# Kernel tuning notes

Measured on AMD Instinct MI355X. Metric: run time of the kernel, lower is better.

Reference implementation:

```python
import jax, jax.numpy as jnp
import numpy as np

N_FFT = 4096
HOP = 1024
EPS = 1e-10


def hann(n):
    # periodic Hann window, matches torch.hann_window(n)
    return 0.5 - 0.5 * jnp.cos(2.0 * jnp.pi * jnp.arange(n) / n)


def stft(x, window):
    # x: (..., T) real -> (..., F, frames) complex; center=True, reflect pad, onesided
    pad = N_FFT // 2
    x = jnp.pad(x, [(0, 0)] * (x.ndim - 1) + [(pad, pad)], mode='reflect')
    n_frames = 1 + (x.shape[-1] - N_FFT) // HOP
    idx = jnp.arange(n_frames)[:, None] * HOP + jnp.arange(N_FFT)[None, :]
    frames = x[..., idx] * window  # (..., frames, N_FFT)
    return jnp.swapaxes(jnp.fft.rfft(frames, axis=-1), -1, -2)  # (..., F, frames)


def istft(spec, window, length):
    # spec: (..., F, frames) complex -> (..., length) real; torch.istft semantics (center=True)
    frames = jnp.fft.irfft(jnp.swapaxes(spec, -1, -2), n=N_FFT, axis=-1) * window
    n_frames = frames.shape[-2]
    out_len = N_FFT + HOP * (n_frames - 1)
    idx = (jnp.arange(n_frames)[:, None] * HOP + jnp.arange(N_FFT)[None, :]).reshape(-1)
    flat = frames.reshape(frames.shape[:-2] + (-1,))
    y = jnp.zeros(frames.shape[:-2] + (out_len,), frames.dtype).at[..., idx].add(flat)
    wsq = jnp.zeros((out_len,), frames.dtype).at[idx].add(jnp.tile(window ** 2, n_frames))
    y = y / jnp.where(wsq > 1e-11, wsq, 1.0)
    pad = N_FFT // 2
    return y[..., pad:pad + length]


def setup_inputs() -> dict:
    key = jax.random.key(0)
    k1, k2, k3 = jax.random.split(key, 3)
    audio = jax.random.normal(k1, (2, 2, 441000), jnp.float32)
    W = jax.random.normal(k2, (4, 2049, 2049), jnp.float32) * 0.02
    b = jax.random.normal(k3, (4, 2049), jnp.float32) * 0.01
    return {"audio": audio, "W": W, "b": b}


def reference(audio, W, b):
    window = hann(N_FFT).astype(audio.dtype)
    mix = stft(audio, window)                 # (N, C, F, T) complex64
    X = jnp.abs(mix)                          # ComplexNorm, mono=False, power=1
    Xd = jax.lax.stop_gradient(X)             # Separator feeds X.detach() to target models
    # target models: per-target linear over frequency bins + ReLU (nonneg spectrogram)
    V = jax.nn.relu(jnp.einsum('ncft,jgf->njcgt', Xd, W) + b[None, :, None, :, None])
    # wiener(iterations=0, softmask=False, residual=False): y_j = v_j * exp(i*angle(mix))
    phase = mix / (jnp.abs(mix) + EPS)        # unit-magnitude complex
    Y = V.astype(phase.real.dtype) * phase[:, None]  # (N, J, C, F, T) complex
    estimates = istft(Y, window, audio.shape[-1])    # (N, J, C, T_audio)
    return estimates
```

## Files before the change

### kernel.cpp

```cpp
#include <hip/hip_runtime.h>
#include <hip/hip_bf16.h>
#include <math.h>

#define T_AUDIO 441000
#define NH   2048
#define HOP  1024
#define NBINS 2049
#define NFRAMES 431
#define PAD  2048

#define GP  2176
#define KP  2112
#define TPN 448

#define NBLK 108
#define SPAN 7168

#define NSTFT (4 * NFRAMES)
#define NCONV ((4 * GP * KP / 8 + 255) / 256)

#define TWO_PI 6.2831853071795864769f

#define PADI(i) ((i) + ((i) >> 4))

typedef __bf16 bf16_t;
typedef bf16_t bf16x8 __attribute__((ext_vector_type(8)));
typedef bf16_t bf16x4 __attribute__((ext_vector_type(4)));
typedef float f32x4 __attribute__((ext_vector_type(4)));
typedef float f32x4u __attribute__((ext_vector_type(4), aligned(4)));
typedef _Float16 h16;
typedef h16 h16x2 __attribute__((ext_vector_type(2)));

__device__ __forceinline__ unsigned pack_bf2(float a, float b) {
    union { bf16_t h; unsigned short u; } ca, cb;
    ca.h = (bf16_t)a; cb.h = (bf16_t)b;
    return (unsigned)ca.u | ((unsigned)cb.u << 16);
}
__device__ __forceinline__ float2 unpack_bf2(unsigned v) {
    union { unsigned u; float f; } a, b;
    a.u = v << 16;
    b.u = v & 0xffff0000u;
    return make_float2(a.f, b.f);
}

__device__ __forceinline__ float2 cadd(float2 a, float2 b) { return make_float2(a.x + b.x, a.y + b.y); }
__device__ __forceinline__ float2 csub(float2 a, float2 b) { return make_float2(a.x - b.x, a.y - b.y); }
__device__ __forceinline__ float2 cmul(float2 a, float2 b) {
    return make_float2(a.x * b.x - a.y * b.y, a.x * b.y + a.y * b.x);
}
__device__ __forceinline__ float2 cmulc(float2 u, float2 w) {
    return make_float2(u.x * w.x + u.y * w.y, u.y * w.x - u.x * w.y);
}

__global__ void k_tab(float2* __restrict__ tw) {
    int i = blockIdx.x * 256 + threadIdx.x;
    if (i < 4096) {
        float s, c;
        sincosf((float)i * (TWO_PI / 4096.0f), &s, &c);
        tw[i] = make_float2(c, s);
    }
}


__device__ __forceinline__ void load_own(float2 v[8], const float2* x, int tid) {
    #pragma unroll
    for (int k = 0; k < 8; k++) v[k] = x[PADI(tid + 256 * k)];
}

template<bool FWD>
__device__ __forceinline__ void r8_sweep_store(const float2 v[8], float2* x,
        int tid, int s, int ls, int fac, const float2* __restrict__ tw) {
    const float sgn = FWD ? -1.0f : 1.0f;
    const float R2 = 0.70710678118654752440f;
    int q = tid & (s - 1);
    int p = tid >> ls;
    int e = p * fac;
    float2 w[7];
    #pragma unroll
    for (int k = 0; k < 7; k++) w[k] = tw[e * (k + 1)];
    float2 s0 = cadd(v[0], v[4]), s1 = cadd(v[1], v[5]),
           s2 = cadd(v[2], v[6]), s3 = cadd(v[3], v[7]);
    float2 d0 = csub(v[0], v[4]), d1 = csub(v[1], v[5]),
           d2 = csub(v[2], v[6]), d3 = csub(v[3], v[7]);
    float2 X0, X1, X2, X3, X4, X5, X6, X7;
    {
        float2 t0 = cadd(s0, s2), t1 = csub(s0, s2);
        float2 t2 = cadd(s1, s3), t3 = csub(s1, s3);
        float2 it3 = make_float2(-sgn * t3.y, sgn * t3.x);
        X0 = cadd(t0, t2); X4 = csub(t0, t2);
        X2 = cadd(t1, it3); X6 = csub(t1, it3);
    }
    {
        float2 e0 = d0;
        float2 e1 = make_float2(R2 * (d1.x - sgn * d1.y), R2 * (sgn * d1.x + d1.y));
        float2 e2 = make_float2(-sgn * d2.y, sgn * d2.x);
        float2 e3 = make_float2(-R2 * (d3.x + sgn * d3.y), R2 * (sgn * d3.x - d3.y));
        float2 t0 = cadd(e0, e2), t1 = csub(e0, e2);
        float2 t2 = cadd(e1, e3), t3 = csub(e1, e3);
        float2 it3 = make_float2(-sgn * t3.y, sgn * t3.x);
        X1 = cadd(t0, t2); X5 = csub(t0, t2);
        X3 = cadd(t1, it3); X7 = csub(t1, it3);
    }
    int ob = q + 8 * s * p;
    x[PADI(ob)] = X0;
    float2 XX[7] = {X1, X2, X3, X4, X5, X6, X7};
    #pragma unroll
    for (int k = 0; k < 7; k++) {
        float2 u = XX[k];
        x[PADI(ob + s * (k + 1))] = FWD ? cmulc(u, w[k]) : cmul(w[k], u);
    }
}

__device__ __forceinline__ void r4_final_reg(const float2 v[8], float2 o[8],
                                             float sgn) {
    #pragma unroll
    for (int h = 0; h < 2; h++) {
        float2 c0 = v[h], c1 = v[h + 2], c2 = v[h + 4], c3 = v[h + 6];
        float2 t0 = cadd(c0, c2), t1 = csub(c0, c2);
        float2 t2 = cadd(c1, c3), t3 = csub(c1, c3);
        float2 it3 = make_float2(-sgn * t3.y, sgn * t3.x);
        o[h]     = cadd(t0, t2);
        o[h + 2] = cadd(t1, it3);
        o[h + 4] = csub(t0, t2);
        o[h + 6] = csub(t1, it3);
    }
}

template<bool FWD>
__device__ __forceinline__ void fft_mid(float2 v[8], float2* buf, int tid,
                                        const float2* __restrict__ tw) {
    r8_sweep_store<FWD>(v, buf, tid, 1, 0, 2, tw);
    __syncthreads();
    load_own(v, buf, tid);
    __syncthreads();
    r8_sweep_store<FWD>(v, buf, tid, 8, 3, 16, tw);
    __syncthreads();
    load_own(v, buf, tid);
    __syncthreads();
    r8_sweep_store<FWD>(v, buf, tid, 64, 6, 128, tw);
    __syncthreads();
    load_own(v, buf, tid);
    __syncthreads();
}

__global__ __launch_bounds__(256) void k_prep(const float* __restrict__ audio,
        const float* __restrict__ W, bf16_t* __restrict__ Wb,
        bf16_t* __restrict__ Xb, unsigned* __restrict__ ph,
        const float2* __restrict__ tw) {
    __shared__ float2 buf[2176];
    int bid = blockIdx.x;
    int tid = threadIdx.x;
    if (bid >= NSTFT) {
        size_t idx = (size_t)(bid - NSTFT) * 256 + tid;
        size_t total = (size_t)4 * GP * KP / 8;
        if (idx >= total) return;
        size_t e = idx * 8;
        int f0 = (int)(e % KP);
        size_t rem = e / KP;
        int g = (int)(rem % GP);
        int j = (int)(rem / GP);
        bf16x8 v = {};
        if (g < NBINS) {
            const float* src = W + ((size_t)j * NBINS + g) * NBINS;
            if (f0 + 7 < NBINS) {
                f32x4u a0 = *(const f32x4u*)(src + f0);
                f32x4u a1 = *(const f32x4u*)(src + f0 + 4);
                #pragma unroll
                for (int r = 0; r < 4; r++) { v[r] = (bf16_t)a0[r]; v[r + 4] = (bf16_t)a1[r]; }
            } else {
                #pragma unroll
                for (int r = 0; r < 8; r++) {
                    int f = f0 + r;
                    v[r] = (bf16_t)(f < NBINS ? src[f] : 0.0f);
                }
            }
        }
        *(bf16x8*)(Wb + e) = v;
        return;
    }
    int nc = bid / NFRAMES;
    int fr = bid - nc * NFRAMES;
    const float* a = audio + (size_t)nc * T_AUDIO;
    int base = fr * HOP - PAD;
    float2 v[8];
    #pragma unroll
    for (int it = 0; it < 8; it++) {
        int m = tid + it * 256;
        int r0 = base + 2 * m;
        int r1 = r0 + 1;
        r0 = r0 < 0 ? -r0 : (r0 >= T_AUDIO ? 2 * T_AUDIO - 2 - r0 : r0);
        r1 = r1 < 0 ? -r1 : (r1 >= T_AUDIO ? 2 * T_AUDIO - 2 - r1 : r1);
        float4 tt = ((const float4*)tw)[m];
        v[it] = make_float2(a[r0] * (0.5f - 0.5f * tt.x),
                            a[r1] * (0.5f - 0.5f * tt.z));
    }
    fft_mid<true>(v, buf, tid, tw);
    {
        float2 o[8];
        r4_final_reg(v, o, -1.0f);
        #pragma unroll
        for (int it = 0; it < 8; it++) buf[PADI(tid + 256 * it)] = o[it];
    }
    __syncthreads();
    size_t orow = ((size_t)nc * NFRAMES + fr) * KP;
    bf16_t* Xrow = Xb + ((size_t)nc * TPN + fr) * KP;
    for (int k = tid; k < NBINS; k += 256) {
        float2 Zk = buf[PADI(k & 2047)];
        float2 Zm = buf[PADI((2048 - k) & 2047)];
        float ex = 0.5f * (Zk.x + Zm.x), ey = 0.5f * (Zk.y - Zm.y);
        float ox = 0.5f * (Zk.y + Zm.y), oy = -0.5f * (Zk.x - Zm.x);
        float2 w = tw[k];
        float re = ex + w.x * ox + w.y * oy;
        float im = ey + w.x * oy - w.y * ox;
        float mag = sqrtf(re * re + im * im);
        float inv = 1.0f / (mag + 1e-10f);
        Xrow[k] = (bf16_t)mag;
        ph[orow + k] = pack_bf2(re * inv, im * inv);
    }
}

__global__ __launch_bounds__(256) void k_gemm_mfma(const bf16_t* __restrict__ Wb,
        const float* __restrict__ bias, const bf16_t* __restrict__ Xb,
        bf16_t* __restrict__ V) {
    __shared__ bf16_t As[128 * 64];
    __shared__ bf16_t Bs[64 * 64];
    int id = blockIdx.x;
    int xcd = id & 7, nn = id >> 3;
    int G = xcd + 8 * (nn / 28);
    if (G >= 68) return;
    int m28 = nn % 28;
    int j  = G / 17;
    int g0 = (G % 17) * 128;
    int nc = m28 / 7;
    int t0 = (m28 % 7) * 64;
    const bf16_t* A = Wb + ((size_t)j * GP + g0) * KP;
    const bf16_t* B = Xb + ((size_t)nc * TPN + t0) * KP;
    int tid = threadIdx.x;
    int lane = tid & 63, wid = tid >> 6;
    int wm = wid >> 1, wn = wid & 1;

    const bf16_t* srcA[4];
    #pragma unroll
    for (int i = 0; i < 4; i++) {
        int s = i * 256 + tid;
        int r = s >> 3, cc = (s & 7) ^ (r & 7);
        srcA[i] = A + (size_t)r * KP + cc * 8;
    }
    const bf16_t* srcB[2];
    #pragma unroll
    for (int i = 0; i < 2; i++) {
        int s = i * 256 + tid;
        int r = s >> 3, cc = (s & 7) ^ (r & 7);
        srcB[i] = B + (size_t)r * KP + cc * 8;
    }

    int laneLo = lane & 15, laneHi = lane >> 4;
    int offA[4][2], offB[2][2];
    #pragma unroll
    for (int mm = 0; mm < 4; mm++) {
        int r = wm * 64 + mm * 16 + laneLo;
        #pragma unroll
        for (int kk = 0; kk < 2; kk++) {
            int c = kk * 4 + laneHi;
            offA[mm][kk] = r * 128 + ((c ^ (r & 7)) << 4);
        }
    }
    #pragma unroll
    for (int n = 0; n < 2; n++) {
        int r = wn * 32 + n * 16 + laneLo;
        #pragma unroll
        for (int kk = 0; kk < 2; kk++) {
            int c = kk * 4 + laneHi;
            offB[n][kk] = r * 128 + ((c ^ (r & 7)) << 4);
        }
    }

    f32x4 acc[4][2];
    #pragma unroll
    for (int mm = 0; mm < 4; mm++)
        #pragma unroll
        for (int n = 0; n < 2; n++)
            acc[mm][n] = (f32x4){0.f, 0.f, 0.f, 0.f};

    for (int k0 = 0; k0 < KP; k0 += 64) {
        #pragma unroll
        for (int i = 0; i < 4; i++)
            __builtin_amdgcn_global_load_lds(
                (const __attribute__((address_space(1))) void*)(srcA[i] + k0),
                (__attribute__((address_space(3))) void*)(As + (i * 256 + tid) * 8),
                16, 0, 0);
        #pragma unroll
        for (int i = 0; i < 2; i++)
            __builtin_amdgcn_global_load_lds(
                (const __attribute__((address_space(1))) void*)(srcB[i] + k0),
                (__attribute__((address_space(3))) void*)(Bs + (i * 256 + tid) * 8),
                16, 0, 0);
        __syncthreads();

        bf16x8 af[4][2], bfr[2][2];
        #pragma unroll
        for (int mm = 0; mm < 4; mm++)
            #pragma unroll
            for (int kk = 0; kk < 2; kk++)
                af[mm][kk] = *(const bf16x8*)((const char*)As + offA[mm][kk]);
        #pragma unroll
        for (int n = 0; n < 2; n++)
            #pragma unroll
            for (int kk = 0; kk < 2; kk++)
                bfr[n][kk] = *(const bf16x8*)((const char*)Bs + offB[n][kk]);
        #pragma unroll
        for (int mm = 0; mm < 4; mm++)
            #pragma unroll
            for (int n = 0; n < 2; n++)
                #pragma unroll
                for (int kk = 0; kk < 2; kk++)
                    acc[mm][n] = __builtin_amdgcn_mfma_f32_16x16x32_bf16(
                        af[mm][kk], bfr[n][kk], acc[mm][n], 0, 0, 0);
        __syncthreads();
    }

    int jnc = j * 4 + nc;
    int colT = laneLo;
    int rowB = laneHi * 4;
    #pragma unroll
    for (int n = 0; n < 2; n++) {
        int t = t0 + wn * 32 + n * 16 + colT;
        if (t >= NFRAMES) continue;
        size_t vrow = ((size_t)jnc * NFRAMES + t) * KP;
        #pragma unroll
        for (int mm = 0; mm < 4; mm++) {
            int g = g0 + wm * 64 + mm * 16 + rowB;
            if (g + 3 < NBINS) {
                bf16x4 o;
                #pragma unroll
                for (int r = 0; r < 4; r++)
                    o[r] = (bf16_t)fmaxf(acc[mm][n][r] + bias[j * NBINS + g + r], 0.0f);
                *(bf16x4*)(V + vrow + g) = o;
            } else {
                #pragma unroll
                for (int r = 0; r < 4; r++) {
                    int gg = g + r;
                    if (gg < NBINS)
                        V[vrow + gg] = (bf16_t)fmaxf(acc[mm][n][r] + bias[j * NBINS + gg], 0.0f);
                }
            }
        }
    }
}

__global__ __launch_bounds__(256) void k_istft(const bf16_t* __restrict__ V,
        const unsigned* __restrict__ ph, const float2* __restrict__ tw,
        h16* __restrict__ strips) {
    __shared__ float2 buf[2176];
    int id = blockIdx.x;
    int xcd = id & 7, slot = id >> 3;
    int wgid = xcd * 216 + slot;
    int j = wgid & 3;
    int t4 = wgid >> 2;
    int nc = t4 / NBLK;
    int b  = t4 - nc * NBLK;
    int njc = (nc >> 1) * 8 + j * 2 + (nc & 1);
    int jnc = j * 4 + nc;
    int tid = threadIdx.x;
    const float scale = 1.0f / 2048.0f;
    float2 acc[14];
    #pragma unroll
    for (int u = 0; u < 14; u++) acc[u] = make_float2(0.f, 0.f);

    #pragma unroll
    for (int p = 0; p < 4; p++) {
        int fr = b * 4 + p;
        if (fr < NFRAMES) {
            size_t vrow = ((size_t)jnc * NFRAMES + fr) * KP;
            size_t prow = ((size_t)nc * NFRAMES + fr) * KP;
            float2 v[8];
            #pragma unroll
            for (int it = 0; it < 8; it++) {
                int k = tid + it * 256;
                int km = 2048 - k;
                float vk = (float)V[vrow + k];
                float2 pk = unpack_bf2(ph[prow + k]);
                float vm = (float)V[vrow + km];
                float2 pm = unpack_bf2(ph[prow + km]);
                float2 Yk = make_float2(vk * pk.x, vk * pk.y);
                float2 Ym = make_float2(vm * pm.x, vm * pm.y);
                float ex = 0.5f * (Yk.x + Ym.x), ey = 0.5f * (Yk.y - Ym.y);
                float wx = 0.5f * (Yk.x - Ym.x), wy = 0.5f * (Yk.y + Ym.y);
                float2 w = tw[k];
                float ox_ = w.x * wx - w.y * wy;
                float oy_ = w.x * wy + w.y * wx;
                v[it] = make_float2(ex - oy_, ey + ox_);
            }
            fft_mid<false>(v, buf, tid, tw);
            float2 o[8];
            r4_final_reg(v, o, 1.0f);
            #pragma unroll
            for (int it = 0; it < 8; it++) {
                int m = tid + it * 256;
                float4 tt = ((const float4*)tw)[m];
                acc[2 * p + it].x += o[it].x * scale * (0.5f - 0.5f * tt.x);
                acc[2 * p + it].y += o[it].y * scale * (0.5f - 0.5f * tt.z);
            }
        }
    }
    h16* dst = strips + ((size_t)njc * NBLK + b) * SPAN;
    #pragma unroll
    for (int u = 0; u < 14; u++) {
        h16x2 o = { (h16)acc[u].x, (h16)acc[u].y };
        *(h16x2*)(dst + 512 * u + 2 * tid) = o;
    }
}

__global__ __launch_bounds__(256) void k_final(const h16* __restrict__ strips,
        const float2* __restrict__ tw, float* __restrict__ out) {
    int gidx = blockIdx.x * 256 + threadIdx.x;
    int t = gidx * 2;
    if (t >= T_AUDIO) return;
    int njc = blockIdx.y;
    const h16* S = strips + (size_t)njc * NBLK * SPAN;
    float o[2];
    #pragma unroll
    for (int u = 0; u < 2; u++) {
        int tt = t + u;
        int q = tt + PAD;
        int b1 = q >> 12, o1 = q & 4095;
        float s = 0.f;
        if (b1 < NBLK) s += (float)S[b1 * SPAN + o1];
        if (b1 > 0 && o1 < SPAN - 4096) s += (float)S[(b1 - 1) * SPAN + o1 + 4096];
        float wsq;
        if (tt >= 1024 && tt <= 439295) {
            wsq = 1.5f;
        } else {
            wsq = 0.f;
            int ib = q >> 10;
            #pragma unroll
            for (int d = 0; d < 4; d++) {
                int i = ib - d;
                if (i >= 0 && i < NFRAMES) {
                    int m = q - (i << 10);
                    float w = 0.5f - 0.5f * tw[m].x;
                    wsq += w * w;
                }
            }
            if (!(wsq > 1e-11f)) wsq = 1.f;
        }
        o[u] = s / wsq;
    }
    *(float2*)(out + (size_t)njc * T_AUDIO + t) = make_float2(o[0], o[1]);
}

extern "C" void kernel_launch(void* const* d_in, const int* in_sizes, int n_in,
                              void* d_out, int out_size, void* d_ws, size_t ws_size,
                              hipStream_t stream) {
    const float* audio = (const float*)d_in[0];
    const float* Wm    = (const float*)d_in[1];
    const float* bias  = (const float*)d_in[2];
    float* out = (float*)d_out;
    char* ws = (char*)d_ws;

    size_t szWb  = (size_t)4 * GP * KP * sizeof(bf16_t);
    size_t szXb  = (size_t)4 * TPN * KP * sizeof(bf16_t);
    size_t szPh  = (size_t)4 * NFRAMES * KP * sizeof(unsigned);
    size_t szV   = (size_t)16 * NFRAMES * KP * sizeof(bf16_t);
    size_t szStr = (size_t)16 * NBLK * SPAN * sizeof(h16);
    size_t szTw  = (size_t)4096 * sizeof(float2);

    bf16_t*   Wb    = (bf16_t*)ws;   ws += szWb;
    bf16_t*   Xb    = (bf16_t*)ws;   ws += szXb;
    unsigned* ph    = (unsigned*)ws; ws += szPh;
    bf16_t*   V     = (bf16_t*)ws;   ws += szV;
    h16*      strips= (h16*)ws;      ws += szStr;
    float2*   tw    = (float2*)ws;   ws += szTw;
    if ((size_t)(ws - (char*)d_ws) > ws_size) return;

    hipMemsetAsync(Xb, 0, szXb, stream);

    k_tab<<<dim3(16), 256, 0, stream>>>(tw);
    k_prep<<<dim3(NSTFT + NCONV), 256, 0, stream>>>(audio, Wm, Wb, Xb, ph, tw);
    k_gemm_mfma<<<dim3(72 * 28), 256, 0, stream>>>(Wb, bias, Xb, V);
    k_istft<<<dim3(1728), 256, 0, stream>>>(V, ph, tw, strips);
    k_final<<<dim3((T_AUDIO / 2 + 255) / 256, 16), 256, 0, stream>>>(strips, tw, out);
}
```

Baseline: 209.8 us.

## Stage iSTFT spectrum rows via LDS async loads, drop Xb memset, vectorize audio reads

Removes the separate memset of the padded Xb buffer. Zeroing of padding rows and columns moves into extra k_prep blocks and the tail of each STFT row. Audio frame loads use float2 vector reads when the index is away from the reflect boundaries. k_istft now prefetches each frame's V and phase rows into shared memory with global_load_lds, overlapping the next frame's load with the current FFT, at the cost of extra LDS and an added barrier.

```diff
diff --git a/kernel.cpp b/kernel.cpp
--- a/kernel.cpp
+++ b/kernel.cpp
@@ -18,6 +18,7 @@
 
 #define NSTFT (4 * NFRAMES)
 #define NCONV ((4 * GP * KP / 8 + 255) / 256)
+#define NPREP (NSTFT + NCONV + 4)
 
 #define TWO_PI 6.2831853071795864769f
 
@@ -151,6 +152,14 @@
     int bid = blockIdx.x;
     int tid = threadIdx.x;
     if (bid >= NSTFT) {
+        if (bid >= NSTFT + NCONV) {
+            int nc = bid - NSTFT - NCONV;
+            bf16_t* dst = Xb + ((size_t)nc * TPN + NFRAMES) * KP;
+            bf16x8 z = {};
+            for (int i = tid; i < (TPN - NFRAMES) * KP / 8; i += 256)
+                *(bf16x8*)(dst + (size_t)i * 8) = z;
+            return;
+        }
         size_t idx = (size_t)(bid - NSTFT) * 256 + tid;
         size_t total = (size_t)4 * GP * KP / 8;
         if (idx >= total) return;
@@ -186,13 +195,18 @@
     #pragma unroll
     for (int it = 0; it < 8; it++) {
         int m = tid + it * 256;
-        int r0 = base + 2 * m;
-        int r1 = r0 + 1;
-        r0 = r0 < 0 ? -r0 : (r0 >= T_AUDIO ? 2 * T_AUDIO - 2 - r0 : r0);
-        r1 = r1 < 0 ? -r1 : (r1 >= T_AUDIO ? 2 * T_AUDIO - 2 - r1 : r1);
         float4 tt = ((const float4*)tw)[m];
-        v[it] = make_float2(a[r0] * (0.5f - 0.5f * tt.x),
-                            a[r1] * (0.5f - 0.5f * tt.z));
+        float w0 = 0.5f - 0.5f * tt.x, w1 = 0.5f - 0.5f * tt.z;
+        int x0 = base + 2 * m;
+        if (x0 >= 0 && x0 + 1 < T_AUDIO) {
+            float2 av = *(const float2*)(a + x0);
+            v[it] = make_float2(av.x * w0, av.y * w1);
+        } else {
+            int r0 = x0, r1 = x0 + 1;
+            r0 = r0 < 0 ? -r0 : (r0 >= T_AUDIO ? 2 * T_AUDIO - 2 - r0 : r0);
+            r1 = r1 < 0 ? -r1 : (r1 >= T_AUDIO ? 2 * T_AUDIO - 2 - r1 : r1);
+            v[it] = make_float2(a[r0] * w0, a[r1] * w1);
+        }
     }
     fft_mid<true>(v, buf, tid, tw);
     {
@@ -217,6 +231,7 @@
         Xrow[k] = (bf16_t)mag;
         ph[orow + k] = pack_bf2(re * inv, im * inv);
     }
+    for (int k = NBINS + tid; k < KP; k += 256) Xrow[k] = (bf16_t)0.0f;
 }
 
 __global__ __launch_bounds__(256) void k_gemm_mfma(const bf16_t* __restrict__ Wb,
@@ -352,6 +367,9 @@
         const unsigned* __restrict__ ph, const float2* __restrict__ tw,
         h16* __restrict__ strips) {
     __shared__ float2 buf[2176];
+    __shared__ __align__(16) unsigned char stg[12336];
+    bf16_t*   Vs = (bf16_t*)stg;
+    unsigned* Ps = (unsigned*)(stg + 4112);
     int id = blockIdx.x;
     int xcd = id & 7, slot = id >> 3;
     int wgid = xcd * 216 + slot;
@@ -367,21 +385,45 @@
     #pragma unroll
     for (int u = 0; u < 14; u++) acc[u] = make_float2(0.f, 0.f);
 
+#define STAGE_F(fr_)                                                           \
+    {                                                                          \
+        const bf16_t* vsrc = V + ((size_t)jnc * NFRAMES + (fr_)) * KP;         \
+        const unsigned* psrc = ph + ((size_t)nc * NFRAMES + (fr_)) * KP;       \
+        __builtin_amdgcn_global_load_lds(                                      \
+            (const __attribute__((address_space(1))) void*)(vsrc + tid * 8),   \
+            (__attribute__((address_space(3))) void*)(Vs + tid * 8), 16, 0, 0);\
+        __builtin_amdgcn_global_load_lds(                                      \
+            (const __attribute__((address_space(1))) void*)(psrc + tid * 4),   \
+            (__attribute__((address_space(3))) void*)(Ps + tid * 4), 16, 0, 0);\
+        __builtin_amdgcn_global_load_lds(                                      \
+            (const __attribute__((address_space(1))) void*)(psrc + 1024 + tid * 4), \
+            (__attribute__((address_space(3))) void*)(Ps + 1024 + tid * 4), 16, 0, 0); \
+        if (tid == 0) {                                                        \
+            __builtin_amdgcn_global_load_lds(                                  \
+                (const __attribute__((address_space(1))) void*)(vsrc + 2048),  \
+                (__attribute__((address_space(3))) void*)(Vs + 2048), 16, 0, 0); \
+            __builtin_amdgcn_global_load_lds(                                  \
+                (const __attribute__((address_space(1))) void*)(psrc + 2048),  \
+                (__attribute__((address_space(3))) void*)(Ps + 2048), 16, 0, 0); \
+        }                                                                      \
+    }
+
+    STAGE_F(b * 4);
+    __syncthreads();
+
     #pragma unroll
     for (int p = 0; p < 4; p++) {
         int fr = b * 4 + p;
         if (fr < NFRAMES) {
-            size_t vrow = ((size_t)jnc * NFRAMES + fr) * KP;
-            size_t prow = ((size_t)nc * NFRAMES + fr) * KP;
             float2 v[8];
             #pragma unroll
             for (int it = 0; it < 8; it++) {
                 int k = tid + it * 256;
                 int km = 2048 - k;
-                float vk = (float)V[vrow + k];
-                float2 pk = unpack_bf2(ph[prow + k]);
-                float vm = (float)V[vrow + km];
-                float2 pm = unpack_bf2(ph[prow + km]);
+                float vk = (float)Vs[k];
+                float2 pk = unpack_bf2(Ps[k]);
+                float vm = (float)Vs[km];
+                float2 pm = unpack_bf2(Ps[km]);
                 float2 Yk = make_float2(vk * pk.x, vk * pk.y);
                 float2 Ym = make_float2(vm * pm.x, vm * pm.y);
                 float ex = 0.5f * (Yk.x + Ym.x), ey = 0.5f * (Yk.y - Ym.y);
@@ -391,6 +433,8 @@
                 float oy_ = w.x * wy + w.y * wx;
                 v[it] = make_float2(ex - oy_, ey + ox_);
             }
+            __syncthreads();
+            if (p < 3) STAGE_F(fr + 1);
             fft_mid<false>(v, buf, tid, tw);
             float2 o[8];
             r4_final_reg(v, o, 1.0f);
@@ -403,6 +447,7 @@
             }
         }
     }
+#undef STAGE_F
     h16* dst = strips + ((size_t)njc * NBLK + b) * SPAN;
     #pragma unroll
     for (int u = 0; u < 14; u++) {
@@ -473,10 +518,8 @@
     float2*   tw    = (float2*)ws;   ws += szTw;
     if ((size_t)(ws - (char*)d_ws) > ws_size) return;
 
-    hipMemsetAsync(Xb, 0, szXb, stream);
-
     k_tab<<<dim3(16), 256, 0, stream>>>(tw);
-    k_prep<<<dim3(NSTFT + NCONV), 256, 0, stream>>>(audio, Wm, Wb, Xb, ph, tw);
+    k_prep<<<dim3(NPREP), 256, 0, stream>>>(audio, Wm, Wb, Xb, ph, tw);
     k_gemm_mfma<<<dim3(72 * 28), 256, 0, stream>>>(Wb, bias, Xb, V);
     k_istft<<<dim3(1728), 256, 0, stream>>>(V, ph, tw, strips);
     k_final<<<dim3((T_AUDIO / 2 + 255) / 256, 16), 256, 0, stream>>>(strips, tw, out);
```

Result: no change. 206.6 us (median of 2 runs) (-1.5%).
